# Kernel optimization log

Measured on AMD Instinct MI355X. Metric: run time of the kernel, lower is better.

Reference implementation:

```python
import jax, jax.numpy as jnp
import numpy as np

N_PROT, N_SUB = 50000, 2000
D_PROT, D_SUB, D_PROJ, KERNEL, N_INT = 256, 256, 128, 16, 64


def setup_inputs() -> dict:
    key = jax.random.key(0)
    ks = jax.random.split(key, 8)
    init = lambda k, shape: jax.random.normal(k, shape, dtype=jnp.float32) * 0.02
    return {
        "prot_node": jax.random.normal(ks[0], (N_PROT, D_PROT), dtype=jnp.float32),
        "sub_node": jax.random.normal(ks[1], (N_SUB, D_SUB), dtype=jnp.float32),
        "int_index": jax.random.randint(ks[2], (N_INT,), 0, N_SUB),
        "Wp": init(ks[3], (D_PROT, D_PROJ)),  # prot_proj weight (in,out layout)
        "bp": jnp.zeros((D_PROJ,), jnp.float32),
        "Ws": init(ks[4], (D_SUB, D_PROJ)),   # sub_proj weight
        "bs": jnp.zeros((D_PROJ,), jnp.float32),
        "wa": init(ks[5], (2 * D_PROJ,)),     # attention_proj weight (out dim 1)
        "ba": jnp.zeros((), jnp.float32),
        "sub_out": init(ks[6], (D_PROJ, D_SUB)),
        "prot_out": init(ks[7], (D_PROJ, D_PROT)),
    }


def reference(prot_node, sub_node, int_index, Wp, bp, Ws, bs, wa, ba, sub_out, prot_out):
    K = KERNEL
    prot_proj = prot_node @ Wp + bp                              # [N, D]
    # reaction potion: sum of projected interacting substrate nodes -> [D]
    reaction = jnp.sum(sub_node[int_index] @ Ws + bs, axis=0)
    num_windows = prot_node.shape[0] - K + 1                     # W
    # attention_proj(concat(window_row, reaction)) splits linearly:
    #   logit = window_row . wa[:D] + reaction . wa[D:] + ba
    # The reaction part is a per-row constant -> compute per-node logits once.
    w1, w2 = wa[:D_PROJ], wa[D_PROJ:]
    g = prot_proj @ w1 + (reaction @ w2 + ba)                    # [N]
    # sliding-window gather indices [W, K]
    idx = jnp.arange(num_windows)[:, None] + jnp.arange(K)[None, :]
    attn = jax.nn.softmax(g[idx], axis=1)                        # [W, K] softmax over window
    local = jnp.einsum('wk,wkd->wd', attn, prot_proj[idx])       # [W, D]
    scores = local + reaction                                    # [W, D]
    # rank windows and pick the best
    top = jnp.argmax(jnp.sum(scores, axis=1))
    top_score = scores[top]                                      # [D]
    # scatter updates back into the node features
    # (set matches torch's non-accumulating fancy-index += for duplicate indices;
    #  the added delta is identical for every row anyway)
    sub_new = sub_node.at[int_index].set(sub_node[int_index] + top_score @ sub_out)
    prot_delta = top_score @ prot_out                            # [D_PROT]
    win = jax.lax.dynamic_slice(prot_node, (top, 0), (K, D_PROT))
    prot_new = jax.lax.dynamic_update_slice(prot_node, win + prot_delta, (top, 0))
    return prot_new, sub_new, int_index
```

## Files before the change

### kernel.cpp

```cpp
#include <hip/hip_runtime.h>
#include <math.h>

#define N_PROT 50000
#define N_SUB  2000
#define D_PROT 256
#define D_SUB  256
#define D_PROJ 128
#define KW     16
#define N_INT  64
#define NWIN   (N_PROT - KW + 1)

#define OUT_SUB (N_PROT * D_PROT)
#define OUT_IDX (OUT_SUB + N_SUB * D_SUB)

#define WS_PACK  0
#define WS_REACT 2
#define WS_CNT   130
#define WS_G     644
#define WS_P     (WS_G + N_PROT)

#define PB 782
#define SB 8
#define NBLK (PB + SB + 1)
#define WBLK ((NWIN + 255) / 256)

__global__ __launch_bounds__(256) void k_main(
    const float* __restrict__ prot, const float* __restrict__ sub_node,
    const int* __restrict__ int_index, const float* __restrict__ Wp,
    const float* __restrict__ Ws, const float* __restrict__ bs,
    const float* __restrict__ wa, float* __restrict__ out,
    float* __restrict__ ws) {
  const int tid = threadIdx.x, lane = tid & 63, wave = tid >> 6;
  const int b = blockIdx.x;
  if (b < PB) {
    __shared__ float su1[D_PROT], su2[D_PROT];
    __shared__ float swa[D_PROJ];
    if (tid < D_PROJ) swa[tid] = wa[tid];
    __syncthreads();
    {
      float s1 = 0.f, s2 = 0.f;
      const float4* wrow = (const float4*)&Wp[tid * D_PROJ];
      #pragma unroll 8
      for (int j4 = 0; j4 < D_PROJ / 4; ++j4) {
        float4 w = wrow[j4];
        float4 a = *(const float4*)&swa[j4 * 4];
        s1 = fmaf(w.x, a.x, fmaf(w.y, a.y, fmaf(w.z, a.z, fmaf(w.w, a.w, s1))));
        s2 += w.x + w.y + w.z + w.w;
      }
      su1[tid] = s1; su2[tid] = s2;
    }
    __syncthreads();
    const float4 c1 = *(const float4*)&su1[lane * 4];
    const float4 c2 = *(const float4*)&su2[lane * 4];
    const int rbase = b * 64 + wave * 16;
    if (rbase + 16 <= N_PROT) {
      #pragma unroll 4
      for (int i = 0; i < 16; ++i) {
        const int r = rbase + i;
        const float4 av = *(const float4*)&prot[r * D_PROT + lane * 4];
        *(float4*)&out[r * D_PROT + lane * 4] = av;
        float g = av.x * c1.x + av.y * c1.y + av.z * c1.z + av.w * c1.w;
        float p = av.x * c2.x + av.y * c2.y + av.z * c2.z + av.w * c2.w;
        #pragma unroll
        for (int off = 32; off > 0; off >>= 1) {
          g += __shfl_xor(g, off, 64);
          p += __shfl_xor(p, off, 64);
        }
        if (lane == 0) { ws[WS_G + r] = g; ws[WS_P + r] = p; }
      }
    } else {
      for (int i = 0; i < 16; ++i) {
        const int r = rbase + i;
        if (r >= N_PROT) break;
        const float4 av = *(const float4*)&prot[r * D_PROT + lane * 4];
        *(float4*)&out[r * D_PROT + lane * 4] = av;
        float g = av.x * c1.x + av.y * c1.y + av.z * c1.z + av.w * c1.w;
        float p = av.x * c2.x + av.y * c2.y + av.z * c2.z + av.w * c2.w;
        for (int off = 32; off > 0; off >>= 1) {
          g += __shfl_xor(g, off, 64);
          p += __shfl_xor(p, off, 64);
        }
        if (lane == 0) { ws[WS_G + r] = g; ws[WS_P + r] = p; }
      }
    }
  } else if (b < PB + SB) {
    const int sb = b - PB;
    #pragma unroll 4
    for (int i = tid; i < 16000; i += 256) {
      const int gi = sb * 16000 + i;
      *(float4*)&out[OUT_SUB + gi * 4] = *(const float4*)&sub_node[gi * 4];
    }
    if (sb == 0 && tid < N_INT) out[OUT_IDX + tid] = (float)int_index[tid];
  } else {
    __shared__ int   ridx[N_INT];
    __shared__ float ssum[D_SUB];
    if (tid < N_INT) ridx[tid] = int_index[tid];
    __syncthreads();
    float acc = 0.f;
    #pragma unroll 8
    for (int i = 0; i < N_INT; ++i) acc += sub_node[ridx[i] * D_SUB + tid];
    ssum[tid] = acc;
    __syncthreads();
    if (tid < D_PROJ) {
      float r = 64.0f * bs[tid];
      #pragma unroll 8
      for (int d = 0; d < D_SUB; ++d) r = fmaf(ssum[d], Ws[d * D_PROJ + tid], r);
      ws[WS_REACT + tid] = r;
    }
    if (tid == 0) {
      *((unsigned long long*)ws) = 0ull;
      ((unsigned int*)ws)[WS_CNT] = 0u;
    }
  }
}

__global__ __launch_bounds__(256) void k_finish(
    const float* __restrict__ prot, const float* __restrict__ sub_node,
    const int* __restrict__ int_index, const float* __restrict__ Wp,
    const float* __restrict__ bp, const float* __restrict__ sub_out,
    const float* __restrict__ prot_out, float* __restrict__ ws,
    float* __restrict__ out) {
  __shared__ float sg[256 + KW], sp[256 + KW];
  __shared__ unsigned long long wred[4];
  __shared__ int slast;
  const int tid = threadIdx.x;
  const int w0 = blockIdx.x * 256;
  for (int i = tid; i < 256 + KW - 1; i += 256) {
    int idx = w0 + i;
    bool ok = idx < N_PROT;
    sg[i] = ok ? ws[WS_G + idx] : -1e30f;
    sp[i] = ok ? ws[WS_P + idx] : 0.f;
  }
  __syncthreads();
  {
    int w = w0 + tid;
    unsigned long long best = 0ull;
    if (w < NWIN) {
      float m = sg[tid];
      #pragma unroll
      for (int k = 1; k < KW; ++k) m = fmaxf(m, sg[tid + k]);
      float s = 0.f, t = 0.f;
      #pragma unroll
      for (int k = 0; k < KW; ++k) {
        float e = expf(sg[tid + k] - m);
        s += e;
        t = fmaf(e, sp[tid + k], t);
      }
      t /= s;
      unsigned int bb = __float_as_uint(t);
      unsigned int u = bb ^ ((bb & 0x80000000u) ? 0xFFFFFFFFu : 0x80000000u);
      best = ((unsigned long long)u << 32) |
             (unsigned long long)(0xFFFFFFFFu - (unsigned)w);
    }
    #pragma unroll
    for (int off = 32; off > 0; off >>= 1) {
      unsigned long long o = __shfl_xor(best, off, 64);
      if (o > best) best = o;
    }
    if ((tid & 63) == 0) wred[tid >> 6] = best;
  }
  __syncthreads();
  if (tid == 0) {
    unsigned long long b2 = wred[0];
    for (int i = 1; i < 4; ++i) if (wred[i] > b2) b2 = wred[i];
    atomicMax((unsigned long long*)ws, b2);
    __threadfence();
    unsigned int ticket = atomicAdd(&((unsigned int*)ws)[WS_CNT], 1u);
    slast = (ticket == WBLK - 1) ? 1 : 0;
  }
  __syncthreads();
  if (!slast) return;

  __shared__ float aprot[KW][D_PROT];
  __shared__ float proj16[KW][D_PROJ];
  __shared__ float attn[KW];
  __shared__ float ts[D_PROJ];
  __shared__ float pdelta[D_PROT], sdelta[D_SUB];
  __shared__ int   sidx[N_INT];
  __shared__ int   swtop;
  if (tid == 0) {
    unsigned long long pk = atomicMax((unsigned long long*)ws, 0ull);
    swtop = (int)(0xFFFFFFFFu - (unsigned)(pk & 0xFFFFFFFFull));
  }
  __syncthreads();
  const int wtop = swtop;
  if (tid < N_INT) sidx[tid] = int_index[tid];
  for (int i = tid; i < KW * D_PROT; i += 256) {
    int rr = i >> 8, dd = i & 255;
    aprot[rr][dd] = prot[(wtop + rr) * D_PROT + dd];
  }
  __syncthreads();
  const int j = tid & 127, half = tid >> 7;
  float accr[8];
  #pragma unroll
  for (int rr = 0; rr < 8; ++rr) accr[rr] = bp[j];
  for (int k = 0; k < D_PROT; ++k) {
    float wv = Wp[k * D_PROJ + j];
    #pragma unroll
    for (int rr = 0; rr < 8; ++rr)
      accr[rr] = fmaf(aprot[half * 8 + rr][k], wv, accr[rr]);
  }
  #pragma unroll
  for (int rr = 0; rr < 8; ++rr) proj16[half * 8 + rr][j] = accr[rr];
  __syncthreads();
  if (tid == 0) {
    float m = ws[WS_G + wtop];
    for (int k = 1; k < KW; ++k) m = fmaxf(m, ws[WS_G + wtop + k]);
    float e[KW], s = 0.f;
    for (int k = 0; k < KW; ++k) { e[k] = expf(ws[WS_G + wtop + k] - m); s += e[k]; }
    for (int k = 0; k < KW; ++k) attn[k] = e[k] / s;
  }
  __syncthreads();
  if (tid < D_PROJ) {
    float a = ws[WS_REACT + tid];
    #pragma unroll
    for (int k = 0; k < KW; ++k) a = fmaf(attn[k], proj16[k][tid], a);
    ts[tid] = a;
  }
  __syncthreads();
  {
    float pa = 0.f, sa = 0.f;
    #pragma unroll 8
    for (int jj = 0; jj < D_PROJ; ++jj) {
      float t = ts[jj];
      pa = fmaf(t, prot_out[jj * D_PROT + tid], pa);
      sa = fmaf(t, sub_out[jj * D_SUB + tid], sa);
    }
    pdelta[tid] = pa; sdelta[tid] = sa;
  }
  __syncthreads();
  for (int i = tid; i < KW * D_PROT; i += 256) {
    int rr = i >> 8, dd = i & 255;
    out[(wtop + rr) * D_PROT + dd] = aprot[rr][dd] + pdelta[dd];
  }
  for (int i = 0; i < N_INT; ++i) {
    int idx = sidx[i];
    out[OUT_SUB + idx * D_SUB + tid] = sub_node[idx * D_SUB + tid] + sdelta[tid];
  }
}

extern "C" void kernel_launch(void* const* d_in, const int* in_sizes, int n_in,
                              void* d_out, int out_size, void* d_ws, size_t ws_size,
                              hipStream_t stream) {
  const float* prot     = (const float*)d_in[0];
  const float* sub      = (const float*)d_in[1];
  const int*   idx      = (const int*)d_in[2];
  const float* Wp       = (const float*)d_in[3];
  const float* bp       = (const float*)d_in[4];
  const float* Ws       = (const float*)d_in[5];
  const float* bs       = (const float*)d_in[6];
  const float* wa       = (const float*)d_in[7];
  const float* sub_out  = (const float*)d_in[9];
  const float* prot_out = (const float*)d_in[10];
  float* out = (float*)d_out;
  float* ws  = (float*)d_ws;

  k_main<<<NBLK, 256, 0, stream>>>(prot, sub, idx, Wp, Ws, bs, wa, out, ws);
  k_finish<<<WBLK, 256, 0, stream>>>(prot, sub, idx, Wp, bp, sub_out, prot_out,
                                     ws, out);
}
```

Before: 187.4 us.

## Hoist weight-vector precompute into prep kernel and widen streaming grid

The per-block recomputation of the Wp·wa and Wp row-sum vectors moves into a separate two-block prep kernel, which also takes over the reaction computation. The main kernel then only streams rows, with smaller blocks (8 rows per wave, 1563 blocks) and all eight loads issued before the stores for more memory-level parallelism. The substrate copy is spread over 64 blocks instead of 8. The cost is one extra kernel launch with a serial dependency before the main pass.

Result: faster. 178.0 us (-5.0%).

```diff
diff --git a/kernel.cpp b/kernel.cpp
--- a/kernel.cpp
+++ b/kernel.cpp
@@ -16,60 +16,94 @@
 #define WS_PACK  0
 #define WS_REACT 2
 #define WS_CNT   130
+#define WS_U1    132
+#define WS_U2    388
 #define WS_G     644
 #define WS_P     (WS_G + N_PROT)
 
-#define PB 782
-#define SB 8
-#define NBLK (PB + SB + 1)
+#define PB 1563
+#define SB 64
+#define NBLK (PB + SB)
 #define WBLK ((NWIN + 255) / 256)
+
+__global__ __launch_bounds__(256) void k_prep(
+    const float* __restrict__ sub_node, const int* __restrict__ int_index,
+    const float* __restrict__ Ws, const float* __restrict__ bs,
+    const float* __restrict__ Wp, const float* __restrict__ wa,
+    float* __restrict__ ws) {
+  const int tid = threadIdx.x;
+  if (blockIdx.x == 0) {
+    __shared__ int   sidx[N_INT];
+    __shared__ float ssum[D_SUB];
+    if (tid < N_INT) sidx[tid] = int_index[tid];
+    __syncthreads();
+    float acc = 0.f;
+    #pragma unroll 8
+    for (int i = 0; i < N_INT; ++i) acc += sub_node[sidx[i] * D_SUB + tid];
+    ssum[tid] = acc;
+    __syncthreads();
+    if (tid < D_PROJ) {
+      float r = 64.0f * bs[tid];
+      #pragma unroll 8
+      for (int d = 0; d < D_SUB; ++d) r = fmaf(ssum[d], Ws[d * D_PROJ + tid], r);
+      ws[WS_REACT + tid] = r;
+    }
+    if (tid == 0) {
+      *((unsigned long long*)ws) = 0ull;
+      ((unsigned int*)ws)[WS_CNT] = 0u;
+    }
+  } else {
+    __shared__ float swa[D_PROJ];
+    if (tid < D_PROJ) swa[tid] = wa[tid];
+    __syncthreads();
+    float s1 = 0.f, s2 = 0.f;
+    const float4* wrow = (const float4*)&Wp[tid * D_PROJ];
+    #pragma unroll 8
+    for (int j4 = 0; j4 < D_PROJ / 4; ++j4) {
+      float4 w = wrow[j4];
+      float4 a = *(const float4*)&swa[j4 * 4];
+      s1 = fmaf(w.x, a.x, fmaf(w.y, a.y, fmaf(w.z, a.z, fmaf(w.w, a.w, s1))));
+      s2 += w.x + w.y + w.z + w.w;
+    }
+    ws[WS_U1 + tid] = s1;
+    ws[WS_U2 + tid] = s2;
+  }
+}
 
 __global__ __launch_bounds__(256) void k_main(
     const float* __restrict__ prot, const float* __restrict__ sub_node,
-    const int* __restrict__ int_index, const float* __restrict__ Wp,
-    const float* __restrict__ Ws, const float* __restrict__ bs,
-    const float* __restrict__ wa, float* __restrict__ out,
+    const int* __restrict__ int_index, float* __restrict__ out,
     float* __restrict__ ws) {
   const int tid = threadIdx.x, lane = tid & 63, wave = tid >> 6;
   const int b = blockIdx.x;
   if (b < PB) {
-    __shared__ float su1[D_PROT], su2[D_PROT];
-    __shared__ float swa[D_PROJ];
-    if (tid < D_PROJ) swa[tid] = wa[tid];
-    __syncthreads();
-    {
-      float s1 = 0.f, s2 = 0.f;
-      const float4* wrow = (const float4*)&Wp[tid * D_PROJ];
-      #pragma unroll 8
-      for (int j4 = 0; j4 < D_PROJ / 4; ++j4) {
-        float4 w = wrow[j4];
-        float4 a = *(const float4*)&swa[j4 * 4];
-        s1 = fmaf(w.x, a.x, fmaf(w.y, a.y, fmaf(w.z, a.z, fmaf(w.w, a.w, s1))));
-        s2 += w.x + w.y + w.z + w.w;
-      }
-      su1[tid] = s1; su2[tid] = s2;
-    }
-    __syncthreads();
-    const float4 c1 = *(const float4*)&su1[lane * 4];
-    const float4 c2 = *(const float4*)&su2[lane * 4];
-    const int rbase = b * 64 + wave * 16;
-    if (rbase + 16 <= N_PROT) {
-      #pragma unroll 4
-      for (int i = 0; i < 16; ++i) {
-        const int r = rbase + i;
-        const float4 av = *(const float4*)&prot[r * D_PROT + lane * 4];
-        *(float4*)&out[r * D_PROT + lane * 4] = av;
-        float g = av.x * c1.x + av.y * c1.y + av.z * c1.z + av.w * c1.w;
-        float p = av.x * c2.x + av.y * c2.y + av.z * c2.z + av.w * c2.w;
+    const float4 c1 = *(const float4*)&ws[WS_U1 + lane * 4];
+    const float4 c2 = *(const float4*)&ws[WS_U2 + lane * 4];
+    const int rbase = b * 32 + wave * 8;
+    if (rbase + 8 <= N_PROT) {
+      float4 av[8];
+      #pragma unroll
+      for (int i = 0; i < 8; ++i)
+        av[i] = *(const float4*)&prot[(rbase + i) * D_PROT + lane * 4];
+      #pragma unroll
+      for (int i = 0; i < 8; ++i)
+        *(float4*)&out[(rbase + i) * D_PROT + lane * 4] = av[i];
+      #pragma unroll
+      for (int i = 0; i < 8; ++i) {
+        float g = av[i].x * c1.x + av[i].y * c1.y + av[i].z * c1.z + av[i].w * c1.w;
+        float p = av[i].x * c2.x + av[i].y * c2.y + av[i].z * c2.z + av[i].w * c2.w;
         #pragma unroll
         for (int off = 32; off > 0; off >>= 1) {
           g += __shfl_xor(g, off, 64);
           p += __shfl_xor(p, off, 64);
         }
-        if (lane == 0) { ws[WS_G + r] = g; ws[WS_P + r] = p; }
+        if (lane == 0) {
+          const int r = rbase + i;
+          ws[WS_G + r] = g; ws[WS_P + r] = p;
+        }
       }
     } else {
-      for (int i = 0; i < 16; ++i) {
+      for (int i = 0; i < 8; ++i) {
         const int r = rbase + i;
         if (r >= N_PROT) break;
         const float4 av = *(const float4*)&prot[r * D_PROT + lane * 4];
@@ -83,34 +117,15 @@
         if (lane == 0) { ws[WS_G + r] = g; ws[WS_P + r] = p; }
       }
     }
-  } else if (b < PB + SB) {
+  } else {
     const int sb = b - PB;
-    #pragma unroll 4
-    for (int i = tid; i < 16000; i += 256) {
-      const int gi = sb * 16000 + i;
-      *(float4*)&out[OUT_SUB + gi * 4] = *(const float4*)&sub_node[gi * 4];
+    #pragma unroll
+    for (int i = 0; i < 8; ++i) {
+      const int gi = sb * 2048 + i * 256 + tid;
+      if (gi < (N_SUB * D_SUB) / 4)
+        *(float4*)&out[OUT_SUB + gi * 4] = *(const float4*)&sub_node[gi * 4];
     }
     if (sb == 0 && tid < N_INT) out[OUT_IDX + tid] = (float)int_index[tid];
-  } else {
-    __shared__ int   ridx[N_INT];
-    __shared__ float ssum[D_SUB];
-    if (tid < N_INT) ridx[tid] = int_index[tid];
-    __syncthreads();
-    float acc = 0.f;
-    #pragma unroll 8
-    for (int i = 0; i < N_INT; ++i) acc += sub_node[ridx[i] * D_SUB + tid];
-    ssum[tid] = acc;
-    __syncthreads();
-    if (tid < D_PROJ) {
-      float r = 64.0f * bs[tid];
-      #pragma unroll 8
-      for (int d = 0; d < D_SUB; ++d) r = fmaf(ssum[d], Ws[d * D_PROJ + tid], r);
-      ws[WS_REACT + tid] = r;
-    }
-    if (tid == 0) {
-      *((unsigned long long*)ws) = 0ull;
-      ((unsigned int*)ws)[WS_CNT] = 0u;
-    }
   }
 }
 
@@ -255,7 +270,8 @@
   float* out = (float*)d_out;
   float* ws  = (float*)d_ws;
 
-  k_main<<<NBLK, 256, 0, stream>>>(prot, sub, idx, Wp, Ws, bs, wa, out, ws);
+  k_prep<<<2, 256, 0, stream>>>(sub, idx, Ws, bs, Wp, wa, ws);
+  k_main<<<NBLK, 256, 0, stream>>>(prot, sub, idx, out, ws);
   k_finish<<<WBLK, 256, 0, stream>>>(prot, sub, idx, Wp, bp, sub_out, prot_out,
                                      ws, out);
 }
```
